# Performance work log

Hardware: AMD Instinct MI355X
Metric: run time of the kernel (lower is better)

Reference implementation:

```python
import jax, jax.numpy as jnp
import numpy as np

N_EMBED = 1024
SEQ_LEN = 2048
BATCH = 4


def setup_inputs() -> dict:
    key = jax.random.key(0)
    ks = jax.random.split(key, 9)
    E = N_EMBED
    x = jax.random.normal(ks[0], (BATCH, SEQ_LEN, E), dtype=jnp.float32)
    s = 0.02
    return {
        "x": x,
        "Wq": jax.random.normal(ks[1], (E, E), dtype=jnp.float32) * s,
        "bq": jnp.zeros((E,), dtype=jnp.float32),
        "Wk": jax.random.normal(ks[2], (E, E), dtype=jnp.float32) * s,
        "bk": jnp.zeros((E,), dtype=jnp.float32),
        "Wv": jax.random.normal(ks[3], (E, E), dtype=jnp.float32) * s,
        "bv": jnp.zeros((E,), dtype=jnp.float32),
        "Wp": jax.random.normal(ks[4], (E, E), dtype=jnp.float32) * s,
        "bp": jnp.zeros((E,), dtype=jnp.float32),
    }


def reference(x, Wq, bq, Wk, bk, Wv, bv, Wp, bp):
    # x: [B, S, E]. Original torch code unpacks (B, C, N) = x.shape and
    # scales by sqrt(C) == sqrt(seq_len)  (a bug we faithfully replicate).
    B, S, E = x.shape
    q = jnp.einsum('bse,fe->bsf', x, Wq) + bq
    k = jnp.einsum('bse,fe->bsf', x, Wk) + bk
    v = jnp.einsum('bse,fe->bsf', x, Wv) + bv
    scale = 1.0 / jnp.sqrt(jnp.asarray(S, dtype=x.dtype))
    scores = jnp.einsum('bqe,bke->bqk', q, k) * scale  # [B, S, S]
    # NOTE: original calls masked_fill (non-inplace) and discards the result,
    # so NO causal mask is actually applied. Replicate that: plain softmax.
    w = jax.nn.softmax(scores, axis=-1)
    o = jnp.einsum('bqk,bke->bqe', w, v)
    out = jnp.einsum('bse,fe->bsf', o, Wp) + bp
    return out
```

## Files before the change

kernel.cpp:

```cpp
#include <hip/hip_runtime.h>


typedef __bf16 bf16x8 __attribute__((ext_vector_type(8)));
typedef float  f32x4  __attribute__((ext_vector_type(4)));
typedef unsigned short u16x8 __attribute__((ext_vector_type(8)));

__device__ __forceinline__ float bf2f(unsigned short u) {
  return __uint_as_float(((unsigned int)u) << 16);
}
__device__ __forceinline__ unsigned short f2bf(float f) {
  unsigned int u = __float_as_uint(f);
  return (unsigned short)((u + 0x7fffu + ((u >> 16) & 1u)) >> 16);
}
__device__ __forceinline__ void gload16(const void* g, void* l) {
  __builtin_amdgcn_global_load_lds(
      (const __attribute__((address_space(1))) void*)g,
      (__attribute__((address_space(3))) void*)l, 16, 0, 0);
}

template <int EPI>
__device__ __forceinline__ void gemm_core(
    char* lds, int nwg, int base,
    const unsigned short* __restrict__ A, const unsigned short* __restrict__ B,
    void* __restrict__ C, const float* __restrict__ bias,
    const float* __restrict__ rowsum,
    int K, long long sA, long long sB, long long sC,
    int nbm, int nbn, int ldc, float scale) {
  char* ldsA = lds;
  char* ldsB = lds + 98304;

  int id = (int)blockIdx.x - base;
  id = (id & 7) * (nwg >> 3) + (id >> 3);
  const int nbmn = nbm * nbn;
  const int bz = id / nbmn;
  const int rem = id - bz * nbmn;
  const int bm = rem / nbn;
  const int bn = rem - bm * nbn;
  const int gm0 = bm * 256, gn0 = bn * 128;

  const unsigned short* Ag = A + (size_t)bz * sA;
  const unsigned short* Bg = B + (size_t)bz * sB;

  const int tid = threadIdx.x;
  const int w = tid >> 6, l = tid & 63;
  const int wr = w >> 1, wc = w & 1;
  const int lr = l & 15;
  const int lk16 = (l >> 4) * 16;
  const int swz = (lr & 7) << 4;

  const int srow = tid >> 3;
  const int sbo  = ((tid & 7) * 16) ^ ((srow & 7) << 4);
  const int sdst = tid * 16;

#define STG_A2(region, ktile, half)                                            \
  do {                                                                         \
    const char* _b =                                                           \
        (const char*)(Ag + (size_t)(gm0 + srow + (half) * 128) * K) +          \
        (size_t)(ktile) * 128 + sbo;                                           \
    const size_t _rk = (size_t)64 * K * 2;                                     \
    gload16(_b,       (region) + (half) * 16384 + sdst);                       \
    gload16(_b + _rk, (region) + (half) * 16384 + 8192 + sdst);                \
  } while (0)
#define STG_B(region, ktile)                                                   \
  do {                                                                         \
    const char* _b = (const char*)(Bg + (size_t)(gn0 + srow) * K) +            \
                     (size_t)(ktile) * 128 + sbo;                              \
    const size_t _rk = (size_t)64 * K * 2;                                     \
    gload16(_b,       (region) + sdst);                                        \
    gload16(_b + _rk, (region) + 8192 + sdst);                                 \
  } while (0)

#define RD_A(dst, m, kh)                                                       \
  dst = *(const bf16x8*)(Abuf + (wr * 64 + (m) * 16 + lr) * 128 +              \
                         ((lk16 + (kh) * 64) ^ swz))
#define RD_B(dst, n, kh)                                                       \
  dst = *(const bf16x8*)(Bbuf + (wc * 64 + (n) * 16 + lr) * 128 +              \
                         ((lk16 + (kh) * 64) ^ swz))

#define LGKM_PIN()                                          \
  asm volatile("s_waitcnt lgkmcnt(0)" ::: "memory");        \
  __builtin_amdgcn_sched_barrier(0)

#define MFMA8(mi0, mi1)                                                        \
  __builtin_amdgcn_s_setprio(1);                                               \
  _Pragma("unroll")                                                            \
  for (int n = 0; n < 4; ++n) {                                                \
    acc[mi0][n] = __builtin_amdgcn_mfma_f32_16x16x32_bf16(a0, bfr[n],          \
                                                          acc[mi0][n], 0,0,0); \
    acc[mi1][n] = __builtin_amdgcn_mfma_f32_16x16x32_bf16(a1, bfr[n],          \
                                                          acc[mi1][n], 0,0,0); \
  }                                                                            \
  __builtin_amdgcn_s_setprio(0)

  f32x4 acc[4][4];
#pragma unroll
  for (int i = 0; i < 4; ++i)
#pragma unroll
    for (int j = 0; j < 4; ++j) acc[i][j] = (f32x4){0.f, 0.f, 0.f, 0.f};

  const int nt = K >> 6;

  STG_B(ldsB, 0); STG_A2(ldsA, 0, 0); STG_A2(ldsA, 0, 1);
  if (nt > 1) {
    STG_B(ldsB + 16384, 1);
    STG_A2(ldsA + 32768, 1, 0); STG_A2(ldsA + 32768, 1, 1);
  }
  if (nt > 1) { asm volatile("s_waitcnt vmcnt(6)" ::: "memory"); }
  else        { asm volatile("s_waitcnt vmcnt(0)" ::: "memory"); }
  __builtin_amdgcn_s_barrier();

  int cur = 0;
  for (int t = 0; t < nt; ++t) {
    char* Abuf = ldsA + cur * 32768;
    char* Bbuf = ldsB + cur * 16384;
    const int nx2 = (cur + 2 >= 3) ? cur - 1 : cur + 2;
    const bool pf = (t + 2 < nt);

    bf16x8 a0, a1, bfr[4];
    RD_A(a0, 0, 0); RD_A(a1, 1, 0);
#pragma unroll
    for (int n = 0; n < 4; ++n) RD_B(bfr[n], n, 0);
    if (pf) STG_B(ldsB + nx2 * 16384, t + 2);
    __builtin_amdgcn_s_barrier();
    LGKM_PIN();
    MFMA8(0, 1);
    __builtin_amdgcn_s_barrier();

    RD_A(a0, 2, 0); RD_A(a1, 3, 0);
    if (pf) STG_A2(ldsA + nx2 * 32768, t + 2, 0);
    __builtin_amdgcn_s_barrier();
    LGKM_PIN();
    MFMA8(2, 3);
    __builtin_amdgcn_s_barrier();

    RD_A(a0, 0, 1); RD_A(a1, 1, 1);
#pragma unroll
    for (int n = 0; n < 4; ++n) RD_B(bfr[n], n, 1);
    if (pf) STG_A2(ldsA + nx2 * 32768, t + 2, 1);
    __builtin_amdgcn_s_barrier();
    LGKM_PIN();
    MFMA8(0, 1);
    __builtin_amdgcn_s_barrier();

    RD_A(a0, 2, 1); RD_A(a1, 3, 1);
    __builtin_amdgcn_s_barrier();
    LGKM_PIN();
    MFMA8(2, 3);
    if (pf)              { asm volatile("s_waitcnt vmcnt(6)" ::: "memory"); }
    else if (t + 1 < nt) { asm volatile("s_waitcnt vmcnt(0)" ::: "memory"); }
    __builtin_amdgcn_s_barrier();

    cur = (cur + 1 >= 3) ? 0 : cur + 1;
  }

  const int cr = (l >> 4) * 4;
  const int cc = l & 15;
#pragma unroll
  for (int m = 0; m < 4; ++m) {
    const int row = gm0 + wr * 64 + m * 16 + cr;
    if constexpr (EPI == 3) {
      const float* rs = rowsum + bz * 2048 + row;
      const f32x4 rv = *(const f32x4*)rs;
      f32x4 inv;
#pragma unroll
      for (int j = 0; j < 4; ++j) inv[j] = 1.0f / rv[j];
      float* Cp = (float*)C + (size_t)bz * sC;
#pragma unroll
      for (int n = 0; n < 4; ++n) {
        const int col = gn0 + wc * 64 + n * 16 + cc;
        const float b = bias[col];
        f32x4 a = acc[m][n];
#pragma unroll
        for (int j = 0; j < 4; ++j)
          Cp[(size_t)(row + j) * ldc + col] = a[j] * inv[j] + b;
      }
    } else {
      unsigned short* Cp = (unsigned short*)C + (size_t)bz * sC;
#pragma unroll
      for (int n = 0; n < 4; ++n) {
        const int col = gn0 + wc * 64 + n * 16 + cc;
        f32x4 a = acc[m][n];
#pragma unroll
        for (int j = 0; j < 4; ++j) {
          float v;
          if constexpr (EPI == 1)      v = a[j] * scale;
          else if constexpr (EPI == 4) v = a[j] + bias[row + j];
          else                         v = a[j] + bias[col];
          Cp[(size_t)(row + j) * ldc + col] = f2bf(v);
        }
      }
    }
  }
#undef STG_A2
#undef STG_B
#undef RD_A
#undef RD_B
#undef LGKM_PIN
#undef MFMA8
}

__global__ __launch_bounds__(256) void prep1(
    const float* __restrict__ wq, const float* __restrict__ wk,
    const float* __restrict__ wv, const float* __restrict__ wp,
    unsigned short* __restrict__ qt, unsigned short* __restrict__ kt,
    unsigned short* __restrict__ vt, unsigned short* __restrict__ wp_bf,
    float* __restrict__ rowsum) {
  const int tid = threadIdx.x;
  if (blockIdx.x >= 1280) {
    const int i = ((blockIdx.x - 1280) * 256 + tid) * 8;
    *(f32x4*)(rowsum + i) = (f32x4){0.f, 0.f, 0.f, 0.f};
    *(f32x4*)(rowsum + i + 4) = (f32x4){0.f, 0.f, 0.f, 0.f};
    return;
  }
  if (blockIdx.x >= 768) {
    const int i = ((blockIdx.x - 768) * 256 + tid) * 8;
    f32x4 a = *(const f32x4*)(wp + i);
    f32x4 b = *(const f32x4*)(wp + i + 4);
    u16x8 o;
    o[0] = f2bf(a[0]); o[1] = f2bf(a[1]); o[2] = f2bf(a[2]); o[3] = f2bf(a[3]);
    o[4] = f2bf(b[0]); o[5] = f2bf(b[1]); o[6] = f2bf(b[2]); o[7] = f2bf(b[3]);
    *(u16x8*)(wp_bf + i) = o;
    return;
  }
  const float* in;
  unsigned short* out;
  int b = blockIdx.x;
  if (b < 256)      { in = wq; out = qt; }
  else if (b < 512) { in = wk; out = kt; b -= 256; }
  else              { in = wv; out = vt; b -= 512; }
  const int r0 = (b >> 4) * 64, c0 = (b & 15) * 64;
  __shared__ unsigned short t[64][72];
  const int rr = tid >> 4;
  const int cc4 = (tid & 15) * 4;
#pragma unroll
  for (int p = 0; p < 4; ++p) {
    const int r = rr + p * 16;
    f32x4 v = *(const f32x4*)(in + (size_t)(r0 + r) * 1024 + c0 + cc4);
    t[cc4 + 0][r] = f2bf(v[0]);
    t[cc4 + 1][r] = f2bf(v[1]);
    t[cc4 + 2][r] = f2bf(v[2]);
    t[cc4 + 3][r] = f2bf(v[3]);
  }
  __syncthreads();
  const int wr_ = tid >> 3;
  const int wc8 = (tid & 7) * 8;
#pragma unroll
  for (int p = 0; p < 2; ++p) {
    const int c = wr_ + p * 32;
    u16x8 o;
#pragma unroll
    for (int j = 0; j < 8; ++j) o[j] = t[c][wc8 + j];
    *(u16x8*)(out + (size_t)(c0 + c) * 1024 + r0 + wc8) = o;
  }
}

__global__ __launch_bounds__(512) void prep2(
    const unsigned short* __restrict__ WkT, const unsigned short* __restrict__ WqT,
    const unsigned short* __restrict__ Wp_bf, const unsigned short* __restrict__ WvT,
    unsigned short* __restrict__ HT, unsigned short* __restrict__ G,
    const float* __restrict__ x, unsigned short* __restrict__ x_bf,
    const float* __restrict__ bq, const float* __restrict__ Wk,
    const float* __restrict__ Wp, const float* __restrict__ bv,
    float* __restrict__ c1, float* __restrict__ cv, float scale) {
  __shared__ char lds[147456];
  const int bid = (int)blockIdx.x;
  const int tid = threadIdx.x;
  if (bid < 32) {
    gemm_core<1>(lds, 32, 0, WkT, WqT, HT, nullptr, nullptr,
                 1024, 0, 0, 0, 4, 8, 1024, scale);
  } else if (bid < 64) {
    gemm_core<1>(lds, 32, 32, Wp_bf, WvT, G, nullptr, nullptr,
                 1024, 0, 0, 0, 4, 8, 1024, 1.0f);
  } else if (bid < 224) {
    for (int u = (bid - 64) * 512 + tid; u < 1048576; u += 160 * 512) {
      const int i = u * 8;
      f32x4 a = *(const f32x4*)(x + i);
      f32x4 b = *(const f32x4*)(x + i + 4);
      u16x8 o;
      o[0] = f2bf(a[0]); o[1] = f2bf(a[1]); o[2] = f2bf(a[2]); o[3] = f2bf(a[3]);
      o[4] = f2bf(b[0]); o[5] = f2bf(b[1]); o[6] = f2bf(b[2]); o[7] = f2bf(b[3]);
      *(u16x8*)(x_bf + i) = o;
    }
  } else if (bid < 226) {
    const int e = (bid - 224) * 512 + tid;
    float acc = 0.f;
    for (int f = 0; f < 1024; ++f) acc += bq[f] * Wk[(size_t)f * 1024 + e];
    c1[e] = acc * scale;
  } else {
    const int l = tid & 63;
    for (int e = (bid - 226) * 8 + (tid >> 6); e < 1024; e += 240) {
      float acc = 0.f;
#pragma unroll
      for (int f = l; f < 1024; f += 64) acc += Wp[(size_t)e * 1024 + f] * bv[f];
#pragma unroll
      for (int i = 1; i < 64; i <<= 1) acc += __shfl_xor(acc, i, 64);
      if (l == 0) cv[e] = acc;
    }
  }
}

__global__ __launch_bounds__(512) void gmid(
    const unsigned short* x, const unsigned short* HT, unsigned short* R,
    const float* c1, const unsigned short* G, unsigned short* VWt,
    const float* cv) {
  __shared__ char lds[147456];
  if (blockIdx.x < 256)
    gemm_core<5>(lds, 256, 0, x, HT, R, c1, nullptr,
                 1024, 0, 0, 0, 32, 8, 1024, 0.f);
  else
    gemm_core<4>(lds, 256, 256, G, x, VWt, cv, nullptr,
                 1024, 0, 2097152, 2097152, 4, 16, 2048, 0.f);
}

__global__ __launch_bounds__(512) void gout(
    const unsigned short* E, const unsigned short* VWt, float* out,
    const float* bp, const float* rowsum) {
  __shared__ char lds[147456];
  gemm_core<3>(lds, 256, 0, E, VWt, out, bp, rowsum,
               2048, 4194304, 2097152, 2097152, 8, 8, 1024, 0.f);
}

__global__ __launch_bounds__(512) void gsco8(
    const unsigned short* __restrict__ A, const unsigned short* __restrict__ B,
    unsigned short* __restrict__ C, float* __restrict__ rowsum,
    int K, long long sA, long long sB, long long sC, int nbm, int nbn) {
  __shared__ char lds[131072];
  char* ldsA = lds;
  char* ldsB = lds + 65536;

  const int nwg = (int)gridDim.x;
  int id = (int)blockIdx.x;
  id = (id & 7) * (nwg >> 3) + (id >> 3);
  const int nbmn = nbm * nbn;
  const int bz = id / nbmn;
  const int rem = id - bz * nbmn;
  const int bm = rem / nbn;
  const int bn = rem - bm * nbn;
  const int gm0 = bm * 256, gn0 = bn * 256;

  const unsigned short* Ag = A + (size_t)bz * sA;
  const unsigned short* Bg = B + (size_t)bz * sB;

  const int tid = threadIdx.x;
  const int w = tid >> 6, l = tid & 63;
  const int wr = w >> 2, wc = w & 3;
  const int lr = l & 15;
  const int lk16 = (l >> 4) * 16;
  const int swz = (lr & 7) << 4;

  const int srow0 = (tid * 16) >> 7;
  const int srow1 = srow0 + 64;
  const int sbo   = ((tid * 16) & 127) ^ ((srow0 & 7) << 4);
  const int sdst0 = tid * 16;
  const int sdst1 = tid * 16 + 8192;

#define STAGE(gbase, grow0, region, ktile)                                     \
  do {                                                                         \
    const char* _s0 =                                                          \
        (const char*)((gbase) + (size_t)((grow0) + srow0) * K) +               \
        (ktile) * 128 + sbo;                                                   \
    const char* _s1 =                                                          \
        (const char*)((gbase) + (size_t)((grow0) + srow1) * K) +               \
        (ktile) * 128 + sbo;                                                   \
    gload16(_s0, (region) + sdst0);                                            \
    gload16(_s1, (region) + sdst1);                                            \
  } while (0)

#define RDA(dst, m, kh) \
  dst = *(const bf16x8*)(Areg + ((m) * 16 + lr) * 128 + ((lk16 + (kh) * 64) ^ swz))
#define RDB(dst, n, kh) \
  dst = *(const bf16x8*)(Breg + (((wc & 1) * 64 + (n) * 16 + lr) * 128) + ((lk16 + (kh) * 64) ^ swz))

  f32x4 acc[8][4];
#pragma unroll
  for (int i = 0; i < 8; ++i)
#pragma unroll
    for (int j = 0; j < 4; ++j) acc[i][j] = (f32x4){0.f, 0.f, 0.f, 0.f};

  bf16x8 af[4][2], bf_[4][2];

#define MM(mi, ai, n)                                                          \
  acc[mi][n] = __builtin_amdgcn_mfma_f32_16x16x32_bf16(af[ai][0], bf_[n][0],   \
                                                       acc[mi][n], 0, 0, 0);   \
  acc[mi][n] = __builtin_amdgcn_mfma_f32_16x16x32_bf16(af[ai][1], bf_[n][1],   \
                                                       acc[mi][n], 0, 0, 0)

#define LGKM_PIN()                                          \
  asm volatile("s_waitcnt lgkmcnt(0)" ::: "memory");        \
  __builtin_amdgcn_sched_barrier(0)

  const int nt = K >> 6;

  STAGE(Bg, gn0,       ldsB + 0,     0);
  STAGE(Bg, gn0 + 128, ldsB + 16384, 0);
  STAGE(Ag, gm0,       ldsA + 0,     0);
  STAGE(Ag, gm0 + 128, ldsA + 16384, 0);
  STAGE(Bg, gn0,       ldsB + 32768,         1);
  STAGE(Bg, gn0 + 128, ldsB + 32768 + 16384, 1);
  STAGE(Ag, gm0,       ldsA + 32768,         1);
  asm volatile("s_waitcnt vmcnt(6)" ::: "memory");
  __builtin_amdgcn_s_barrier();

  for (int t = 0; t < nt; ++t) {
    const int cur = t & 1;
    char* Areg  = ldsA + cur * 32768 + wr * 16384;
    char* Breg  = ldsB + cur * 32768 + (wc >> 1) * 16384;
    char* Anext = ldsA + (cur ^ 1) * 32768;
    char* Acur2 = ldsA + cur * 32768;
    char* Bcur2 = ldsB + cur * 32768;

#pragma unroll
    for (int m = 0; m < 4; ++m) { RDA(af[m][0], m, 0); RDA(af[m][1], m, 1); }
#pragma unroll
    for (int n = 0; n < 2; ++n) { RDB(bf_[n][0], n, 0); RDB(bf_[n][1], n, 1); }
    if (wc < 2) {
#pragma unroll
      for (int n = 2; n < 4; ++n) { RDB(bf_[n][0], n, 0); RDB(bf_[n][1], n, 1); }
    }
    if (t + 1 < nt) STAGE(Ag, gm0 + 128, Anext + 16384, t + 1);
    __builtin_amdgcn_s_barrier();
    LGKM_PIN();
    __builtin_amdgcn_s_setprio(1);
    MM(0, 0, 0); MM(0, 0, 1); MM(1, 1, 0); MM(1, 1, 1);
    MM(2, 2, 0); MM(2, 2, 1); MM(3, 3, 0); MM(3, 3, 1);
    __builtin_amdgcn_s_setprio(0);
    __builtin_amdgcn_s_barrier();

    if (wc >= 2) {
#pragma unroll
      for (int n = 2; n < 4; ++n) { RDB(bf_[n][0], n, 0); RDB(bf_[n][1], n, 1); }
    }
    if (t + 2 < nt) STAGE(Bg, gn0, Bcur2, t + 2);
    __builtin_amdgcn_s_barrier();
    LGKM_PIN();
    __builtin_amdgcn_s_setprio(1);
    MM(0, 0, 2); MM(0, 0, 3); MM(1, 1, 2); MM(1, 1, 3);
    MM(2, 2, 2); MM(2, 2, 3); MM(3, 3, 2); MM(3, 3, 3);
    __builtin_amdgcn_s_setprio(0);
    __builtin_amdgcn_s_barrier();

#pragma unroll
    for (int m = 0; m < 4; ++m) { RDA(af[m][0], m + 4, 0); RDA(af[m][1], m + 4, 1); }
    if (t + 2 < nt) STAGE(Bg, gn0 + 128, Bcur2 + 16384, t + 2);
    __builtin_amdgcn_s_barrier();
    LGKM_PIN();
    __builtin_amdgcn_s_setprio(1);
    MM(4, 0, 0); MM(4, 0, 1); MM(5, 1, 0); MM(5, 1, 1);
    MM(6, 2, 0); MM(6, 2, 1); MM(7, 3, 0); MM(7, 3, 1);
    __builtin_amdgcn_s_setprio(0);
    __builtin_amdgcn_s_barrier();

    if (t + 2 < nt) STAGE(Ag, gm0, Acur2, t + 2);
    __builtin_amdgcn_s_barrier();
    __builtin_amdgcn_s_setprio(1);
    MM(4, 0, 2); MM(4, 0, 3); MM(5, 1, 2); MM(5, 1, 3);
    MM(6, 2, 2); MM(6, 2, 3); MM(7, 3, 2); MM(7, 3, 3);
    __builtin_amdgcn_s_setprio(0);
    if (t + 2 < nt) {
      asm volatile("s_waitcnt vmcnt(6)" ::: "memory");
    } else {
      asm volatile("s_waitcnt vmcnt(0)" ::: "memory");
    }
    __builtin_amdgcn_s_barrier();
  }

  const int cr = (l >> 4) * 4;
  const int cc = l & 15;
  unsigned short* Cp = C + (size_t)bz * sC;
#pragma unroll
  for (int m = 0; m < 8; ++m) {
    const int row = gm0 + wr * 128 + m * 16 + cr;
    float psum[4] = {0.f, 0.f, 0.f, 0.f};
#pragma unroll
    for (int n = 0; n < 4; ++n) {
      const int col = gn0 + wc * 64 + n * 16 + cc;
      f32x4 a = acc[m][n];
#pragma unroll
      for (int j = 0; j < 4; ++j) {
        const unsigned short us = f2bf(exp2f(a[j]));
        Cp[(size_t)(row + j) * 2048 + col] = us;
        psum[j] += bf2f(us);
      }
    }
#pragma unroll
    for (int j = 0; j < 4; ++j) {
#pragma unroll
      for (int i = 1; i < 16; i <<= 1) psum[j] += __shfl_xor(psum[j], i, 16);
      if ((l & 15) == 0) atomicAdd(rowsum + bz * 2048 + row + j, psum[j]);
    }
  }
#undef STAGE
#undef RDA
#undef RDB
#undef MM
#undef LGKM_PIN
}

extern "C" void kernel_launch(void* const* d_in, const int* in_sizes, int n_in,
                              void* d_out, int out_size, void* d_ws, size_t ws_size,
                              hipStream_t stream) {
  const float* x  = (const float*)d_in[0];
  const float* Wq = (const float*)d_in[1];
  const float* bq = (const float*)d_in[2];
  const float* Wk = (const float*)d_in[3];
  const float* bk = (const float*)d_in[4];  (void)bk;
  const float* Wv = (const float*)d_in[5];
  const float* bv = (const float*)d_in[6];
  const float* Wp = (const float*)d_in[7];
  const float* bp = (const float*)d_in[8];
  float* out = (float*)d_out;

  char* ws = (char*)d_ws;
  unsigned short* x_bf  = (unsigned short*)(ws);
  unsigned short* Wp_bf = (unsigned short*)(ws + (16ull << 20));
  unsigned short* WqT   = (unsigned short*)(ws + (18ull << 20));
  unsigned short* WkT   = (unsigned short*)(ws + (20ull << 20));
  unsigned short* WvT   = (unsigned short*)(ws + (22ull << 20));
  unsigned short* HT    = (unsigned short*)(ws + (24ull << 20));
  unsigned short* G     = (unsigned short*)(ws + (26ull << 20));
  float*          c1    = (float*)(ws + (28ull << 20));
  float*          cv    = (float*)(ws + (28ull << 20) + 65536);
  unsigned short* R     = (unsigned short*)(ws + (32ull << 20));
  unsigned short* VWt   = (unsigned short*)(ws + (48ull << 20));
  unsigned short* Em    = (unsigned short*)(ws + (64ull << 20));
  float*          rowsum = (float*)(ws + (96ull << 20));

  const float scale_ht = 0.022097086912079608f * 1.4426950408889634f;

  prep1<<<1284, 256, 0, stream>>>(Wq, Wk, Wv, Wp, WqT, WkT, WvT, Wp_bf, rowsum);
  prep2<<<256, 512, 0, stream>>>(WkT, WqT, Wp_bf, WvT, HT, G,
                                 x, x_bf, bq, Wk, Wp, bv, c1, cv, scale_ht);
  gmid<<<512, 512, 0, stream>>>(x_bf, HT, R, c1, G, VWt, cv);
  gsco8<<<256, 512, 0, stream>>>(R, x_bf, Em, rowsum,
                                 1024, 2097152, 2097152, 4194304, 8, 8);
  gout<<<256, 512, 0, stream>>>(Em, VWt, out, bp, rowsum);
}
```

Before: 165.0 us.

## Use smaller-LDS K=32 double-buffered GEMM core in gmid for higher occupancy

Adds a new GEMM core that stages 32-wide K tiles with double buffering in 48KB of LDS instead of the 144KB used by the original core. The gmid kernel now calls this core and declares launch bounds allowing more blocks per CU. The aim is to raise occupancy and hide latency on the two mid GEMMs. In exchange it runs more loop iterations with a barrier each and has a shallower per-iteration MFMA pipeline, so there may be more synchronisation overhead.

```diff
diff --git a/kernel.cpp b/kernel.cpp
--- a/kernel.cpp
+++ b/kernel.cpp
@@ -16,6 +16,124 @@
   __builtin_amdgcn_global_load_lds(
       (const __attribute__((address_space(1))) void*)g,
       (__attribute__((address_space(3))) void*)l, 16, 0, 0);
+}
+
+template <int EPI>
+__device__ __forceinline__ void gemm32_core(
+    char* lds, int nwg, int base,
+    const unsigned short* __restrict__ A, const unsigned short* __restrict__ B,
+    void* __restrict__ C, const float* __restrict__ bias,
+    int K, long long sA, long long sB, long long sC,
+    int nbm, int nbn, int ldc) {
+  char* ldsA = lds;
+  char* ldsB = lds + 32768;
+
+  int id = (int)blockIdx.x - base;
+  id = (id & 7) * (nwg >> 3) + (id >> 3);
+  const int nbmn = nbm * nbn;
+  const int bz = id / nbmn;
+  const int rem = id - bz * nbmn;
+  const int bm = rem / nbn;
+  const int bn = rem - bm * nbn;
+  const int gm0 = bm * 256, gn0 = bn * 128;
+
+  const unsigned short* Ag = A + (size_t)bz * sA;
+  const unsigned short* Bg = B + (size_t)bz * sB;
+
+  const int tid = threadIdx.x;
+  const int w = tid >> 6, l = tid & 63;
+  const int wr = w >> 1, wc = w & 1;
+  const int lr = l & 15;
+  const int rchunk = ((l >> 4) ^ ((lr >> 1) & 3)) << 4;
+
+  const int srow = tid >> 2;
+  const int sbo  = (((tid & 3) ^ ((tid >> 3) & 3)) << 4);
+  const int sdst = tid * 16;
+
+#define STG32_A(bufsel, ktile)                                                 \
+  do {                                                                         \
+    char* _d = ldsA + (bufsel) * 16384 + sdst;                                 \
+    const char* _s0 = (const char*)(Ag + (size_t)(gm0 + srow) * K) +           \
+                      (size_t)(ktile) * 64 + sbo;                              \
+    const char* _s1 = (const char*)(Ag + (size_t)(gm0 + 128 + srow) * K) +     \
+                      (size_t)(ktile) * 64 + sbo;                              \
+    gload16(_s0, _d);                                                          \
+    gload16(_s1, _d + 8192);                                                   \
+  } while (0)
+#define STG32_B(bufsel, ktile)                                                 \
+  do {                                                                         \
+    const char* _s = (const char*)(Bg + (size_t)(gn0 + srow) * K) +            \
+                     (size_t)(ktile) * 64 + sbo;                               \
+    gload16(_s, ldsB + (bufsel) * 8192 + sdst);                                \
+  } while (0)
+
+#define RD32_A(dst, m)                                                         \
+  dst = *(const bf16x8*)(Abuf + (wr * 64 + (m) * 16 + lr) * 64 + rchunk)
+#define RD32_B(dst, n)                                                         \
+  dst = *(const bf16x8*)(Bbuf + (wc * 64 + (n) * 16 + lr) * 64 + rchunk)
+
+  f32x4 acc[4][4];
+#pragma unroll
+  for (int i = 0; i < 4; ++i)
+#pragma unroll
+    for (int j = 0; j < 4; ++j) acc[i][j] = (f32x4){0.f, 0.f, 0.f, 0.f};
+
+  const int nt = K >> 5;
+
+  STG32_A(0, 0); STG32_B(0, 0);
+  asm volatile("s_waitcnt vmcnt(0)" ::: "memory");
+  __builtin_amdgcn_s_barrier();
+
+  for (int t = 0; t < nt; ++t) {
+    const int cur = t & 1;
+    char* Abuf = ldsA + cur * 16384;
+    char* Bbuf = ldsB + cur * 8192;
+    const bool pf = (t + 1 < nt);
+
+    if (pf) { STG32_A(cur ^ 1, t + 1); STG32_B(cur ^ 1, t + 1); }
+
+    bf16x8 av[4], bv[4];
+#pragma unroll
+    for (int m = 0; m < 4; ++m) RD32_A(av[m], m);
+#pragma unroll
+    for (int n = 0; n < 4; ++n) RD32_B(bv[n], n);
+    asm volatile("s_waitcnt lgkmcnt(0)" ::: "memory");
+    __builtin_amdgcn_sched_barrier(0);
+    __builtin_amdgcn_s_setprio(1);
+#pragma unroll
+    for (int m = 0; m < 4; ++m)
+#pragma unroll
+      for (int n = 0; n < 4; ++n)
+        acc[m][n] = __builtin_amdgcn_mfma_f32_16x16x32_bf16(av[m], bv[n],
+                                                            acc[m][n], 0, 0, 0);
+    __builtin_amdgcn_s_setprio(0);
+    if (pf) { asm volatile("s_waitcnt vmcnt(0)" ::: "memory"); }
+    __builtin_amdgcn_s_barrier();
+  }
+
+  const int cr = (l >> 4) * 4;
+  const int cc = l & 15;
+  unsigned short* Cp = (unsigned short*)C + (size_t)bz * sC;
+#pragma unroll
+  for (int m = 0; m < 4; ++m) {
+    const int row = gm0 + wr * 64 + m * 16 + cr;
+#pragma unroll
+    for (int n = 0; n < 4; ++n) {
+      const int col = gn0 + wc * 64 + n * 16 + cc;
+      f32x4 a = acc[m][n];
+#pragma unroll
+      for (int j = 0; j < 4; ++j) {
+        float v;
+        if constexpr (EPI == 4) v = a[j] + bias[row + j];
+        else                    v = a[j] + bias[col];
+        Cp[(size_t)(row + j) * ldc + col] = f2bf(v);
+      }
+    }
+  }
+#undef STG32_A
+#undef STG32_B
+#undef RD32_A
+#undef RD32_B
 }
 
 template <int EPI>
@@ -299,17 +417,17 @@
   }
 }
 
-__global__ __launch_bounds__(512) void gmid(
+__global__ __launch_bounds__(512, 4) void gmid(
     const unsigned short* x, const unsigned short* HT, unsigned short* R,
     const float* c1, const unsigned short* G, unsigned short* VWt,
     const float* cv) {
-  __shared__ char lds[147456];
+  __shared__ char lds[49152];
   if (blockIdx.x < 256)
-    gemm_core<5>(lds, 256, 0, x, HT, R, c1, nullptr,
-                 1024, 0, 0, 0, 32, 8, 1024, 0.f);
+    gemm32_core<5>(lds, 256, 0, x, HT, R, c1,
+                   1024, 0, 0, 0, 32, 8, 1024);
   else
-    gemm_core<4>(lds, 256, 256, G, x, VWt, cv, nullptr,
-                 1024, 0, 2097152, 2097152, 4, 16, 2048, 0.f);
+    gemm32_core<4>(lds, 256, 256, G, x, VWt, cv,
+                   1024, 0, 2097152, 2097152, 4, 16, 2048);
 }
 
 __global__ __launch_bounds__(512) void gout(
```

After: 164.6 us. No clear change (-0.2%).
